# Performance work log

Measured on AMD Instinct MI355X. Metric: run time of the kernel, lower is better.

The kernel has to match this reference:

```python
import jax, jax.numpy as jnp
import numpy as np

FEAT_DIM = 2048
H_DIM = 1024
N = 8192  # num_obj (tree nodes in pre-order traversal order)


def setup_inputs() -> dict:
    key = jax.random.key(0)
    ks = jax.random.split(key, 5)
    features = jax.random.normal(ks[0], (N, FEAT_DIM), dtype=jnp.float32)
    # block_orthogonal init approximated by scaled gaussian (same math at runtime)
    Wx = jax.random.normal(ks[1], (4 * H_DIM, FEAT_DIM), dtype=jnp.float32) / np.sqrt(FEAT_DIM)
    Wh = jax.random.normal(ks[2], (4 * H_DIM, H_DIM), dtype=jnp.float32) / np.sqrt(H_DIM)
    bx = jnp.zeros((4 * H_DIM,), dtype=jnp.float32)
    # iofuh bias: forget-gate block [2h:3h] filled with 1.0
    bh = jnp.zeros((4 * H_DIM,), dtype=jnp.float32).at[2 * H_DIM:3 * H_DIM].set(1.0)
    # binary tree in pre-order-compatible (topological) order: parent of t is (t-1)//2 < t; root = -1
    t = jnp.arange(N)
    parent_idx = jnp.where(t == 0, -1, (t - 1) // 2).astype(jnp.int32)
    root_c = jax.random.normal(ks[3], (1, H_DIM), dtype=jnp.float32)
    root_h = jax.random.normal(ks[4], (1, H_DIM), dtype=jnp.float32)
    return {"features": features, "Wx": Wx, "bx": bx, "Wh": Wh, "bh": bh,
            "parent_idx": parent_idx, "root_c": root_c, "root_h": root_h}


def reference(features, Wx, bx, Wh, bh, parent_idx, root_c, root_h):
    # Precompute the input projection for ALL nodes with one big GEMM
    # (the original does this per-node; math is identical).
    xproj = features @ Wx.T + (bx + bh)  # [N, 4H]
    WhT = Wh.T  # [H, 4H]
    # state buffers; slot 0 holds the root state, slot t+1 holds node t's state
    h_buf = jnp.concatenate([root_h, jnp.zeros((N, H_DIM), features.dtype)], axis=0)  # [N+1, H]
    c_buf = jnp.concatenate([root_c, jnp.zeros((N, H_DIM), features.dtype)], axis=0)

    def step(carry, inp):
        h_buf, c_buf = carry
        t, p, xp = inp
        hp = h_buf[p + 1]  # parent hidden [H]
        cp = c_buf[p + 1]  # parent cell   [H]
        iofu = xp + hp @ WhT  # [4H]
        i, o, f, u = jnp.split(iofu, 4)
        i = jax.nn.sigmoid(i)
        o = jax.nn.sigmoid(o)
        f = jax.nn.sigmoid(f)
        u = jnp.tanh(u)
        c = i * u + f * cp
        h = o * jnp.tanh(c)
        h_buf = h_buf.at[t + 1].set(h)
        c_buf = c_buf.at[t + 1].set(c)
        return (h_buf, c_buf), h

    ts = jnp.arange(N)
    (_, _), hidden = jax.lax.scan(step, (h_buf, c_buf), (ts, parent_idx, xproj))
    return hidden  # [N, H] == treelstm_io.hidden rows in traversal order
```

## Files before the change

kernel.cpp:

```cpp
#include <hip/hip_runtime.h>
#include <hip/hip_fp16.h>
#include <math.h>

#define FEAT 2048
#define HD 1024
#define FH 4096
#define NN 8192

using s16x8 = __attribute__((ext_vector_type(8))) short;
using f32x4 = __attribute__((ext_vector_type(4))) float;

#define GLOBAL_AS __attribute__((address_space(1)))
#define LDS_AS __attribute__((address_space(3)))

__device__ __forceinline__ void gload_lds16(const void* g, void* l) {
    __builtin_amdgcn_global_load_lds((const GLOBAL_AS unsigned int*)g,
                                     (LDS_AS unsigned int*)l, 16, 0, 0);
}

__device__ __forceinline__ unsigned short f2bf(float f) {
    union { float f; unsigned u; } v; v.f = f;
    unsigned r = v.u + 0x7FFFu + ((v.u >> 16) & 1u);
    return (unsigned short)(r >> 16);
}

__device__ __forceinline__ float fast_sig(float x) { return 1.0f / (1.0f + __expf(-x)); }
__device__ __forceinline__ float fast_tanh(float x) {
    float ax = fabsf(x);
    float e = __expf(2.0f * ax);
    float r = 1.0f - 2.0f / (e + 1.0f);
    return copysignf(r, x);
}

__global__ __launch_bounds__(256) void convert_all_kernel(
    const float* __restrict__ feat, const float* __restrict__ Wx,
    const float* __restrict__ Wh, unsigned short* __restrict__ feat_b,
    unsigned short* __restrict__ Wx_b, unsigned short* __restrict__ Wh_b,
    const float* __restrict__ root_h, const float* __restrict__ root_c,
    unsigned short* __restrict__ h_buf, float* __restrict__ c_buf)
{
    const size_t g = (size_t)blockIdx.x * 256 + threadIdx.x;
    if (g < HD) { h_buf[g] = f2bf(root_h[g]); c_buf[g] = root_c[g]; }

    const size_t n1 = (size_t)NN * FEAT;
    const size_t n2 = n1 + (size_t)FH * FEAT;
    size_t i = g * 8;
    const float* s; unsigned short* d;
    if (i < n1)      { s = feat + i;        d = feat_b + i; }
    else if (i < n2) { s = Wx + (i - n1);   d = Wx_b + (i - n1); }
    else             { s = Wh + (i - n2);   d = Wh_b + (i - n2); }
    float4 a = *(const float4*)s;
    float4 b = *(const float4*)(s + 4);
    unsigned short r[8] = {f2bf(a.x), f2bf(a.y), f2bf(a.z), f2bf(a.w),
                           f2bf(b.x), f2bf(b.y), f2bf(b.z), f2bf(b.w)};
    *(s16x8*)d = *(const s16x8*)r;
}

__global__ __launch_bounds__(512, 2) void xproj_8ph(
    const unsigned short* __restrict__ Ab,
    const unsigned short* __restrict__ Bb,
    const float* __restrict__ bx, const float* __restrict__ bh,
    __half* __restrict__ xproj)
{
    __shared__ char lds[131072];
    const int tid = threadIdx.x;
    const int wid = tid >> 6;
    const int lane = tid & 63;
    const int wr = wid >> 2;
    const int wc = wid & 3;
    const int bm = blockIdx.x * 256;
    const int bn = blockIdx.y * 256;
    const int fr = lane & 15;
    const int fq = lane >> 4;

    const int srow = tid >> 3;
    const int sslot = (tid & 7) ^ (srow & 7);
    const unsigned short* gA[4];
    const unsigned short* gB[4];
    #pragma unroll
    for (int q = 0; q < 4; ++q) {
        gA[q] = Ab + (size_t)(bm + q * 64 + srow) * FEAT + sslot * 8;
        gB[q] = Bb + (size_t)(bn + q * 64 + srow) * FEAT + sslot * 8;
    }
    const int ldsoff = tid * 16;

    f32x4 acc[8][4];
    #pragma unroll
    for (int i = 0; i < 8; ++i)
        #pragma unroll
        for (int j = 0; j < 4; ++j) { f32x4 z = {0.f, 0.f, 0.f, 0.f}; acc[i][j] = z; }

    #pragma unroll
    for (int q = 0; q < 4; ++q) {
        gload_lds16(gA[q], lds + q * 8192 + ldsoff);
        gload_lds16(gB[q], lds + 32768 + q * 8192 + ldsoff);
    }

    for (int t = 0; t < 32; ++t) {
        const int d = t & 1;
        const char* LA = lds + d * 65536;
        const char* LB = LA + 32768;
        char* SA = lds + (d ^ 1) * 65536;
        char* SB = SA + 32768;
        const int knext = (t + 1) * 64;

        asm volatile("s_waitcnt vmcnt(0)" ::: "memory");
        __builtin_amdgcn_s_barrier();

        #pragma unroll
        for (int kk = 0; kk < 2; ++kk) {
            const int kbyte = kk * 64 + fq * 16;
            s16x8 aF[8], bF[4];
            #pragma unroll
            for (int i = 0; i < 8; ++i) {
                const int row = wr * 128 + i * 16 + fr;
                aF[i] = *(const s16x8*)(LA + row * 128 + (kbyte ^ ((row & 7) << 4)));
            }
            #pragma unroll
            for (int j = 0; j < 4; ++j) {
                const int row = wc * 64 + j * 16 + fr;
                bF[j] = *(const s16x8*)(LB + row * 128 + (kbyte ^ ((row & 7) << 4)));
            }
            if (t < 31) {
                if (kk == 0) {
                    #pragma unroll
                    for (int q = 0; q < 4; ++q)
                        gload_lds16(gA[q] + knext, SA + q * 8192 + ldsoff);
                } else {
                    #pragma unroll
                    for (int q = 0; q < 4; ++q)
                        gload_lds16(gB[q] + knext, SB + q * 8192 + ldsoff);
                }
            }
            __builtin_amdgcn_s_setprio(1);
            #pragma unroll
            for (int i = 0; i < 8; ++i)
                #pragma unroll
                for (int j = 0; j < 4; ++j)
                    acc[i][j] = __builtin_amdgcn_mfma_f32_16x16x32_bf16(
                        aF[i], bF[j], acc[i][j], 0, 0, 0);
            __builtin_amdgcn_s_setprio(0);
        }
    }

    __builtin_amdgcn_s_barrier();
    char* W = lds + wid * 16384;
    #pragma unroll
    for (int j = 0; j < 4; ++j) {
        const int c_loc = j * 16 + fr;
        const int col = bn + wc * 64 + c_loc;
        const float bias = bx[col] + bh[col];
        #pragma unroll
        for (int i = 0; i < 8; ++i) {
            #pragma unroll
            for (int reg = 0; reg < 4; ++reg) {
                const int r_loc = i * 16 + fq * 4 + reg;
                const int byteo = r_loc * 128 +
                    ((((c_loc >> 3) ^ (r_loc & 7)) << 4)) + (c_loc & 7) * 2;
                *(__half*)(W + byteo) = __float2half_rn(acc[i][j][reg] + bias);
            }
        }
    }
    asm volatile("s_waitcnt lgkmcnt(0)" ::: "memory");
    #pragma unroll
    for (int k = 0; k < 16; ++k) {
        const int f = k * 64 + lane;
        const int r_loc = f >> 3;
        const int cchunk = f & 7;
        const s16x8 v = *(const s16x8*)(W + r_loc * 128 +
                                        ((cchunk ^ (r_loc & 7)) << 4));
        const int grow = bm + wr * 128 + r_loc;
        const int gcol = bn + wc * 64 + cchunk * 8;
        *(s16x8*)((unsigned short*)xproj + (size_t)grow * FH + gcol) = v;
    }
}

template<int BM>
__global__ __launch_bounds__(512, 2) void level_kk(
    const __half* __restrict__ xproj, const unsigned short* __restrict__ Whb,
    int start, int prevstart, unsigned short* __restrict__ h_buf,
    float* __restrict__ c_buf, float* __restrict__ out)
{
    constexpr int MR = BM / 32;
    constexpr int ABYTES = BM * 128;
    constexpr int BUF = ABYTES + 32768;
    __shared__ char lds[2 * BUF];
    const int tid = threadIdx.x;
    const int wid = tid >> 6, lane = tid & 63;
    const int wr = wid >> 2, wc = wid & 3;
    const int fr = lane & 15, fq = lane >> 4;
    const int t0 = start + blockIdx.x * BM;
    const int jg0 = blockIdx.y * 64;

    const int srow = tid >> 3;
    const int sslot = (tid & 7) ^ (srow & 7);
    const unsigned short* gA[BM / 64];
    #pragma unroll
    for (int q = 0; q < BM / 64; ++q) {
        const int rg = blockIdx.x * BM + q * 64 + srow;
        gA[q] = h_buf + (size_t)(prevstart + (rg >> 1) + 1) * HD + sslot * 8;
    }
    const unsigned short* gB[4];
    #pragma unroll
    for (int q = 0; q < 4; ++q) {
        const int r = q * 64 + srow;
        const int whrow = ((r >> 4) & 3) * 1024 + jg0 + ((r >> 6) * 16) + (r & 15);
        gB[q] = Whb + (size_t)whrow * HD + sslot * 8;
    }
    const int ldsoff = tid * 16;

    f32x4 acc[MR][4];
    #pragma unroll
    for (int i = 0; i < MR; ++i)
        #pragma unroll
        for (int j = 0; j < 4; ++j) { f32x4 z = {0.f, 0.f, 0.f, 0.f}; acc[i][j] = z; }

    #pragma unroll
    for (int q = 0; q < BM / 64; ++q)
        gload_lds16(gA[q], lds + q * 8192 + ldsoff);
    #pragma unroll
    for (int q = 0; q < 4; ++q)
        gload_lds16(gB[q], lds + ABYTES + q * 8192 + ldsoff);

    for (int t = 0; t < 16; ++t) {
        const char* LA = lds + (t & 1) * BUF;
        const char* LB = LA + ABYTES;
        char* SA = lds + ((t & 1) ^ 1) * BUF;
        char* SB = SA + ABYTES;
        const int knext = (t + 1) * 64;

        asm volatile("s_waitcnt vmcnt(0)" ::: "memory");
        __builtin_amdgcn_s_barrier();

        #pragma unroll
        for (int kk = 0; kk < 2; ++kk) {
            const int kbyte = kk * 64 + fq * 16;
            s16x8 aF[MR], bF[4];
            #pragma unroll
            for (int i = 0; i < MR; ++i) {
                const int row = wr * (BM / 2) + i * 16 + fr;
                aF[i] = *(const s16x8*)(LA + row * 128 + (kbyte ^ ((row & 7) << 4)));
            }
            #pragma unroll
            for (int j = 0; j < 4; ++j) {
                const int row = wc * 64 + j * 16 + fr;
                bF[j] = *(const s16x8*)(LB + row * 128 + (kbyte ^ ((row & 7) << 4)));
            }
            if (t < 15) {
                if (kk == 0) {
                    #pragma unroll
                    for (int q = 0; q < BM / 64; ++q)
                        gload_lds16(gA[q] + knext, SA + q * 8192 + ldsoff);
                } else {
                    #pragma unroll
                    for (int q = 0; q < 4; ++q)
                        gload_lds16(gB[q] + knext, SB + q * 8192 + ldsoff);
                }
            }
            __builtin_amdgcn_s_setprio(1);
            #pragma unroll
            for (int i = 0; i < MR; ++i)
                #pragma unroll
                for (int j = 0; j < 4; ++j)
                    acc[i][j] = __builtin_amdgcn_mfma_f32_16x16x32_bf16(
                        aF[i], bF[j], acc[i][j], 0, 0, 0);
            __builtin_amdgcn_s_setprio(0);
        }
    }

    const int col = jg0 + wc * 16 + fr;
    #pragma unroll
    for (int i = 0; i < MR; ++i) {
        #pragma unroll
        for (int reg = 0; reg < 4; ++reg) {
            const int t = t0 + wr * (BM / 2) + i * 16 + fq * 4 + reg;
            const int p = (t - 1) >> 1;
            const size_t xb = (size_t)t * FH + col;
            const float gi = acc[i][0][reg] + __half2float(xproj[xb]);
            const float go = acc[i][1][reg] + __half2float(xproj[xb + HD]);
            const float gf = acc[i][2][reg] + __half2float(xproj[xb + 2 * HD]);
            const float gu = acc[i][3][reg] + __half2float(xproj[xb + 3 * HD]);
            const float cp = c_buf[(size_t)(p + 1) * HD + col];
            const float c = fast_sig(gi) * fast_tanh(gu) + fast_sig(gf) * cp;
            const float h = fast_sig(go) * fast_tanh(c);
            c_buf[(size_t)(t + 1) * HD + col] = c;
            h_buf[(size_t)(t + 1) * HD + col] = f2bf(h);
            out[(size_t)t * HD + col] = h;
        }
    }
}

__device__ __forceinline__ void level_epilogue(
    f32x4 (&acc)[4][4], const __half* __restrict__ xproj,
    const int* __restrict__ parent, unsigned short* __restrict__ h_buf,
    float* __restrict__ c_buf, float* __restrict__ out,
    int t0, int lim, int wm, int col, int fq)
{
    #pragma unroll
    for (int i = 0; i < 4; ++i) {
        #pragma unroll
        for (int reg = 0; reg < 4; ++reg) {
            const int t = t0 + wm + i * 16 + fq * 4 + reg;
            if (t < lim) {
                const int p = parent[t];
                const size_t xb = (size_t)t * FH + col;
                const float gi = acc[i][0][reg] + __half2float(xproj[xb]);
                const float go = acc[i][1][reg] + __half2float(xproj[xb + HD]);
                const float gf = acc[i][2][reg] + __half2float(xproj[xb + 2 * HD]);
                const float gu = acc[i][3][reg] + __half2float(xproj[xb + 3 * HD]);
                const float cp = c_buf[(size_t)(p + 1) * HD + col];
                const float c = fast_sig(gi) * fast_tanh(gu) + fast_sig(gf) * cp;
                const float h = fast_sig(go) * fast_tanh(c);
                c_buf[(size_t)(t + 1) * HD + col] = c;
                h_buf[(size_t)(t + 1) * HD + col] = f2bf(h);
                out[(size_t)t * HD + col] = h;
            }
        }
    }
}

__device__ __forceinline__ void bk128_issue(
    const unsigned short* const (&gA)[8], const unsigned short* const (&gB)[8],
    int k0, unsigned short* As, unsigned short* Bs, int wbase)
{
    #pragma unroll
    for (int q = 0; q < 8; ++q) {
        gload_lds16(gA[q] + k0, (char*)As + q * 4096 + wbase);
        gload_lds16(gB[q] + k0, (char*)Bs + q * 4096 + wbase);
    }
}

__device__ __forceinline__ void bk128_compute(
    const unsigned short* As, const unsigned short* Bs,
    f32x4 (&acc)[4][4], int wm, int wn16, int fr, int fkb)
{
    #pragma unroll
    for (int kk = 0; kk < 4; ++kk) {
        s16x8 aF[4], bF[4];
        #pragma unroll
        for (int i = 0; i < 4; ++i) {
            const int r = wm + i * 16 + fr;
            const int byteIn = (kk * 64 + fkb) ^ ((r & 7) << 4);
            aF[i] = *(const s16x8*)((const char*)As + r * 256 + byteIn);
        }
        #pragma unroll
        for (int g = 0; g < 4; ++g) {
            const int r = g * 32 + wn16 + fr;
            const int byteIn = (kk * 64 + fkb) ^ ((r & 7) << 4);
            bF[g] = *(const s16x8*)((const char*)Bs + r * 256 + byteIn);
        }
        #pragma unroll
        for (int i = 0; i < 4; ++i)
            #pragma unroll
            for (int g = 0; g < 4; ++g)
                acc[i][g] = __builtin_amdgcn_mfma_f32_16x16x32_bf16(aF[i], bF[g], acc[i][g], 0, 0, 0);
    }
}

__global__ __launch_bounds__(256) void level_bk128_dbuf(
    const __half* __restrict__ xproj, const unsigned short* __restrict__ Whb,
    const int* __restrict__ parent, unsigned short* __restrict__ h_buf,
    float* __restrict__ c_buf, float* __restrict__ out,
    int start, int count)
{
    __shared__ unsigned short As0[128 * 128];
    __shared__ unsigned short Bs0[128 * 128];
    __shared__ unsigned short As1[128 * 128];
    __shared__ unsigned short Bs1[128 * 128];
    const int tid = threadIdx.x;
    const int wid = tid >> 6;
    const int lane = tid & 63;
    const int t0 = start + blockIdx.x * 128;
    const int jg0 = blockIdx.y * 32;
    const int lim = start + count;
    const int wm = (wid & 1) * 64;
    const int wn16 = (wid >> 1) * 16;
    const int wbase = wid * 1024;
    const int srow_b = tid >> 4;
    const int rowbyte = (tid & 15) * 16;

    const unsigned short* gA[8];
    const unsigned short* gB[8];
    #pragma unroll
    for (int q = 0; q < 8; ++q) {
        const int r = q * 16 + srow_b;
        const int sk = (rowbyte ^ ((r & 7) << 4)) >> 1;
        const int tA = min(t0 + r, lim - 1);
        gA[q] = h_buf + (size_t)(parent[tA] + 1) * HD + sk;
        const int whrow = ((r >> 5) << 10) + jg0 + (r & 31);
        gB[q] = Whb + (size_t)whrow * HD + sk;
    }

    f32x4 acc[4][4];
    #pragma unroll
    for (int i = 0; i < 4; ++i)
        #pragma unroll
        for (int g = 0; g < 4; ++g) { f32x4 z = {0.f, 0.f, 0.f, 0.f}; acc[i][g] = z; }

    const int fr = lane & 15;
    const int fkb = (lane >> 4) * 16;

    bk128_issue(gA, gB, 0, As0, Bs0, wbase);
    #pragma unroll
    for (int t = 0; t < 8; ++t) {
        unsigned short* curA = (t & 1) ? As1 : As0;
        unsigned short* curB = (t & 1) ? Bs1 : Bs0;
        unsigned short* nxtA = (t & 1) ? As0 : As1;
        unsigned short* nxtB = (t & 1) ? Bs0 : Bs1;
        if (t < 7) {
            bk128_issue(gA, gB, (t + 1) * 128, nxtA, nxtB, wbase);
            asm volatile("s_waitcnt vmcnt(16)" ::: "memory");
        } else {
            asm volatile("s_waitcnt vmcnt(0)" ::: "memory");
        }
        __builtin_amdgcn_s_barrier();
        __builtin_amdgcn_sched_barrier(0);
        bk128_compute(curA, curB, acc, wm, wn16, fr, fkb);
        __builtin_amdgcn_sched_barrier(0);
        __builtin_amdgcn_s_barrier();
    }

    level_epilogue(acc, xproj, parent, h_buf, c_buf, out,
                   t0, lim, wm, jg0 + wn16 + fr, lane >> 4);
}

extern "C" void kernel_launch(void* const* d_in, const int* in_sizes, int n_in,
                              void* d_out, int out_size, void* d_ws, size_t ws_size,
                              hipStream_t stream) {
    const float* feat   = (const float*)d_in[0];
    const float* Wx     = (const float*)d_in[1];
    const float* bx     = (const float*)d_in[2];
    const float* Wh     = (const float*)d_in[3];
    const float* bh     = (const float*)d_in[4];
    const int*   parent = (const int*)d_in[5];
    const float* root_c = (const float*)d_in[6];
    const float* root_h = (const float*)d_in[7];
    float* out = (float*)d_out;

    char* ws = (char*)d_ws;
    __half* xproj = (__half*)ws;                        ws += (size_t)NN * FH * 2;
    float* c_buf = (float*)ws;                          ws += (size_t)(NN + 1) * HD * 4;
    unsigned short* feat_b = (unsigned short*)ws;       ws += (size_t)NN * FEAT * 2;
    unsigned short* Wx_b = (unsigned short*)ws;         ws += (size_t)FH * FEAT * 2;
    unsigned short* Wh_b = (unsigned short*)ws;         ws += (size_t)FH * HD * 2;
    unsigned short* h_buf = (unsigned short*)ws;        ws += (size_t)(NN + 1) * HD * 2;

    const size_t ntot = (size_t)NN * FEAT + (size_t)FH * FEAT + (size_t)FH * HD;
    convert_all_kernel<<<(unsigned)(ntot / 8 / 256), 256, 0, stream>>>(
        feat, Wx, Wh, feat_b, Wx_b, Wh_b, root_h, root_c, h_buf, c_buf);

    dim3 g1(NN / 256, FH / 256);
    xproj_8ph<<<g1, 512, 0, stream>>>(feat_b, Wx_b, bx, bh, xproj);

    for (int start = 0, sz = 1; sz <= 512; start += sz, sz *= 2) {
        dim3 g2((sz + 127) / 128, HD / 32);
        level_bk128_dbuf<<<g2, 256, 0, stream>>>(
            xproj, Wh_b, parent, h_buf, c_buf, out, start, sz);
    }

    dim3 gl(16, 16);
    level_kk<64><<<gl, 512, 0, stream>>>(xproj, Wh_b, 1023, 511,
                                         h_buf, c_buf, out);
    level_kk<128><<<gl, 512, 0, stream>>>(xproj, Wh_b, 2047, 1023,
                                          h_buf, c_buf, out);
    level_kk<256><<<gl, 512, 0, stream>>>(xproj, Wh_b, 4095, 2047,
                                          h_buf, c_buf, out);

    dim3 g3(1, HD / 32);
    level_bk128_dbuf<<<g3, 256, 0, stream>>>(
        xproj, Wh_b, parent, h_buf, c_buf, out, 8191, 1);
}
```

Before: 435.1 us.

## Fuse small tree levels into one persistent kernel with atomic level flags

Replaces the ten separate per-level launches for levels 0-9 with a single 224-block kernel. Blocks are assigned to levels and spin on per-level atomic done counters (acquire/release at agent scope) before reading the parent states. This removes launch gaps and tail serialization between the tiny levels. It relies on all 224 blocks being co-resident to avoid deadlock, and spinning blocks occupy CUs while they wait.

```diff
diff --git a/kernel.cpp b/kernel.cpp
--- a/kernel.cpp
+++ b/kernel.cpp
@@ -37,10 +37,12 @@
     const float* __restrict__ Wh, unsigned short* __restrict__ feat_b,
     unsigned short* __restrict__ Wx_b, unsigned short* __restrict__ Wh_b,
     const float* __restrict__ root_h, const float* __restrict__ root_c,
-    unsigned short* __restrict__ h_buf, float* __restrict__ c_buf)
+    unsigned short* __restrict__ h_buf, float* __restrict__ c_buf,
+    int* __restrict__ done)
 {
     const size_t g = (size_t)blockIdx.x * 256 + threadIdx.x;
     if (g < HD) { h_buf[g] = f2bf(root_h[g]); c_buf[g] = root_c[g]; }
+    if (g < 16) done[g] = 0;
 
     const size_t n1 = (size_t)NN * FEAT;
     const size_t n2 = n1 + (size_t)FH * FEAT;
@@ -175,6 +177,147 @@
     }
 }
 
+__global__ __launch_bounds__(512, 2) void levels_fused_small(
+    const __half* __restrict__ xproj, const unsigned short* __restrict__ Whb,
+    unsigned short* __restrict__ h_buf, float* __restrict__ c_buf,
+    float* __restrict__ out, int* __restrict__ done)
+{
+    constexpr int MR = 4;
+    constexpr int ABYTES = 128 * 128;
+    constexpr int BUF = ABYTES + 32768;
+    __shared__ char lds[2 * BUF];
+    const int bid = blockIdx.x;
+    int lvl, nb;
+    if (bid < 128)      { lvl = bid >> 4; nb = 0; }
+    else if (bid < 160) { lvl = 8;        nb = (bid - 128) >> 4; }
+    else                { lvl = 9;        nb = (bid - 160) >> 4; }
+    const int jg0 = (bid & 15) * 64;
+    const int start = (1 << lvl) - 1;
+    const int cnt = 1 << lvl;
+    const int lim = start + cnt;
+    const int t0 = start + nb * 128;
+
+    if (lvl > 0) {
+        if (threadIdx.x == 0) {
+            const int need = (lvl <= 8) ? 16 : 32;
+            while (__hip_atomic_load(done + (lvl - 1), __ATOMIC_ACQUIRE,
+                                     __HIP_MEMORY_SCOPE_AGENT) < need)
+                __builtin_amdgcn_s_sleep(8);
+        }
+        __syncthreads();
+    }
+
+    const int tid = threadIdx.x;
+    const int wid = tid >> 6, lane = tid & 63;
+    const int wr = wid >> 2, wc = wid & 3;
+    const int fr = lane & 15, fq = lane >> 4;
+
+    const int srow = tid >> 3;
+    const int sslot = (tid & 7) ^ (srow & 7);
+    const unsigned short* gA[2];
+    #pragma unroll
+    for (int q = 0; q < 2; ++q) {
+        const int rg = min(nb * 128 + q * 64 + srow, cnt - 1);
+        const int arow = ((start + rg - 1) >> 1) + 1;
+        gA[q] = h_buf + (size_t)arow * HD + sslot * 8;
+    }
+    const unsigned short* gB[4];
+    #pragma unroll
+    for (int q = 0; q < 4; ++q) {
+        const int r = q * 64 + srow;
+        const int whrow = ((r >> 4) & 3) * 1024 + jg0 + ((r >> 6) * 16) + (r & 15);
+        gB[q] = Whb + (size_t)whrow * HD + sslot * 8;
+    }
+    const int ldsoff = tid * 16;
+
+    f32x4 acc[MR][4];
+    #pragma unroll
+    for (int i = 0; i < MR; ++i)
+        #pragma unroll
+        for (int j = 0; j < 4; ++j) { f32x4 z = {0.f, 0.f, 0.f, 0.f}; acc[i][j] = z; }
+
+    #pragma unroll
+    for (int q = 0; q < 2; ++q)
+        gload_lds16(gA[q], lds + q * 8192 + ldsoff);
+    #pragma unroll
+    for (int q = 0; q < 4; ++q)
+        gload_lds16(gB[q], lds + ABYTES + q * 8192 + ldsoff);
+
+    for (int t = 0; t < 16; ++t) {
+        const char* LA = lds + (t & 1) * BUF;
+        const char* LB = LA + ABYTES;
+        char* SA = lds + ((t & 1) ^ 1) * BUF;
+        char* SB = SA + ABYTES;
+        const int knext = (t + 1) * 64;
+
+        asm volatile("s_waitcnt vmcnt(0)" ::: "memory");
+        __builtin_amdgcn_s_barrier();
+
+        #pragma unroll
+        for (int kk = 0; kk < 2; ++kk) {
+            const int kbyte = kk * 64 + fq * 16;
+            s16x8 aF[MR], bF[4];
+            #pragma unroll
+            for (int i = 0; i < MR; ++i) {
+                const int row = wr * 64 + i * 16 + fr;
+                aF[i] = *(const s16x8*)(LA + row * 128 + (kbyte ^ ((row & 7) << 4)));
+            }
+            #pragma unroll
+            for (int j = 0; j < 4; ++j) {
+                const int row = wc * 64 + j * 16 + fr;
+                bF[j] = *(const s16x8*)(LB + row * 128 + (kbyte ^ ((row & 7) << 4)));
+            }
+            if (t < 15) {
+                if (kk == 0) {
+                    #pragma unroll
+                    for (int q = 0; q < 2; ++q)
+                        gload_lds16(gA[q] + knext, SA + q * 8192 + ldsoff);
+                } else {
+                    #pragma unroll
+                    for (int q = 0; q < 4; ++q)
+                        gload_lds16(gB[q] + knext, SB + q * 8192 + ldsoff);
+                }
+            }
+            __builtin_amdgcn_s_setprio(1);
+            #pragma unroll
+            for (int i = 0; i < MR; ++i)
+                #pragma unroll
+                for (int j = 0; j < 4; ++j)
+                    acc[i][j] = __builtin_amdgcn_mfma_f32_16x16x32_bf16(
+                        aF[i], bF[j], acc[i][j], 0, 0, 0);
+            __builtin_amdgcn_s_setprio(0);
+        }
+    }
+
+    const int col = jg0 + wc * 16 + fr;
+    #pragma unroll
+    for (int i = 0; i < MR; ++i) {
+        #pragma unroll
+        for (int reg = 0; reg < 4; ++reg) {
+            const int t = t0 + wr * 64 + i * 16 + fq * 4 + reg;
+            if (t < lim) {
+                const int prow = ((t - 1) >> 1) + 1;
+                const size_t xb = (size_t)t * FH + col;
+                const float gi = acc[i][0][reg] + __half2float(xproj[xb]);
+                const float go = acc[i][1][reg] + __half2float(xproj[xb + HD]);
+                const float gf = acc[i][2][reg] + __half2float(xproj[xb + 2 * HD]);
+                const float gu = acc[i][3][reg] + __half2float(xproj[xb + 3 * HD]);
+                const float cp = c_buf[(size_t)prow * HD + col];
+                const float c = fast_sig(gi) * fast_tanh(gu) + fast_sig(gf) * cp;
+                const float h = fast_sig(go) * fast_tanh(c);
+                c_buf[(size_t)(t + 1) * HD + col] = c;
+                h_buf[(size_t)(t + 1) * HD + col] = f2bf(h);
+                out[(size_t)t * HD + col] = h;
+            }
+        }
+    }
+
+    __syncthreads();
+    if (threadIdx.x == 0)
+        __hip_atomic_fetch_add(done + lvl, 1, __ATOMIC_RELEASE,
+                               __HIP_MEMORY_SCOPE_AGENT);
+}
+
 template<int BM>
 __global__ __launch_bounds__(512, 2) void level_kk(
     const __half* __restrict__ xproj, const unsigned short* __restrict__ Whb,
@@ -286,35 +429,6 @@
             c_buf[(size_t)(t + 1) * HD + col] = c;
             h_buf[(size_t)(t + 1) * HD + col] = f2bf(h);
             out[(size_t)t * HD + col] = h;
-        }
-    }
-}
-
-__device__ __forceinline__ void level_epilogue(
-    f32x4 (&acc)[4][4], const __half* __restrict__ xproj,
-    const int* __restrict__ parent, unsigned short* __restrict__ h_buf,
-    float* __restrict__ c_buf, float* __restrict__ out,
-    int t0, int lim, int wm, int col, int fq)
-{
-    #pragma unroll
-    for (int i = 0; i < 4; ++i) {
-        #pragma unroll
-        for (int reg = 0; reg < 4; ++reg) {
-            const int t = t0 + wm + i * 16 + fq * 4 + reg;
-            if (t < lim) {
-                const int p = parent[t];
-                const size_t xb = (size_t)t * FH + col;
-                const float gi = acc[i][0][reg] + __half2float(xproj[xb]);
-                const float go = acc[i][1][reg] + __half2float(xproj[xb + HD]);
-                const float gf = acc[i][2][reg] + __half2float(xproj[xb + 2 * HD]);
-                const float gu = acc[i][3][reg] + __half2float(xproj[xb + 3 * HD]);
-                const float cp = c_buf[(size_t)(p + 1) * HD + col];
-                const float c = fast_sig(gi) * fast_tanh(gu) + fast_sig(gf) * cp;
-                const float h = fast_sig(go) * fast_tanh(c);
-                c_buf[(size_t)(t + 1) * HD + col] = c;
-                h_buf[(size_t)(t + 1) * HD + col] = f2bf(h);
-                out[(size_t)t * HD + col] = h;
-            }
         }
     }
 }
@@ -420,8 +534,29 @@
         __builtin_amdgcn_s_barrier();
     }
 
-    level_epilogue(acc, xproj, parent, h_buf, c_buf, out,
-                   t0, lim, wm, jg0 + wn16 + fr, lane >> 4);
+    const int col = jg0 + wn16 + fr;
+    const int fq = lane >> 4;
+    #pragma unroll
+    for (int i = 0; i < 4; ++i) {
+        #pragma unroll
+        for (int reg = 0; reg < 4; ++reg) {
+            const int t = t0 + wm + i * 16 + fq * 4 + reg;
+            if (t < lim) {
+                const int p = parent[t];
+                const size_t xb = (size_t)t * FH + col;
+                const float gi = acc[i][0][reg] + __half2float(xproj[xb]);
+                const float go = acc[i][1][reg] + __half2float(xproj[xb + HD]);
+                const float gf = acc[i][2][reg] + __half2float(xproj[xb + 2 * HD]);
+                const float gu = acc[i][3][reg] + __half2float(xproj[xb + 3 * HD]);
+                const float cp = c_buf[(size_t)(p + 1) * HD + col];
+                const float c = fast_sig(gi) * fast_tanh(gu) + fast_sig(gf) * cp;
+                const float h = fast_sig(go) * fast_tanh(c);
+                c_buf[(size_t)(t + 1) * HD + col] = c;
+                h_buf[(size_t)(t + 1) * HD + col] = f2bf(h);
+                out[(size_t)t * HD + col] = h;
+            }
+        }
+    }
 }
 
 extern "C" void kernel_launch(void* const* d_in, const int* in_sizes, int n_in,
@@ -444,19 +579,17 @@
     unsigned short* Wx_b = (unsigned short*)ws;         ws += (size_t)FH * FEAT * 2;
     unsigned short* Wh_b = (unsigned short*)ws;         ws += (size_t)FH * HD * 2;
     unsigned short* h_buf = (unsigned short*)ws;        ws += (size_t)(NN + 1) * HD * 2;
+    int* done = (int*)ws;                               ws += 256;
 
     const size_t ntot = (size_t)NN * FEAT + (size_t)FH * FEAT + (size_t)FH * HD;
     convert_all_kernel<<<(unsigned)(ntot / 8 / 256), 256, 0, stream>>>(
-        feat, Wx, Wh, feat_b, Wx_b, Wh_b, root_h, root_c, h_buf, c_buf);
+        feat, Wx, Wh, feat_b, Wx_b, Wh_b, root_h, root_c, h_buf, c_buf, done);
 
     dim3 g1(NN / 256, FH / 256);
     xproj_8ph<<<g1, 512, 0, stream>>>(feat_b, Wx_b, bx, bh, xproj);
 
-    for (int start = 0, sz = 1; sz <= 512; start += sz, sz *= 2) {
-        dim3 g2((sz + 127) / 128, HD / 32);
-        level_bk128_dbuf<<<g2, 256, 0, stream>>>(
-            xproj, Wh_b, parent, h_buf, c_buf, out, start, sz);
-    }
+    levels_fused_small<<<224, 512, 0, stream>>>(
+        xproj, Wh_b, h_buf, c_buf, out, done);
 
     dim3 gl(16, 16);
     level_kk<64><<<gl, 512, 0, stream>>>(xproj, Wh_b, 1023, 511,
```

Measured after the change: 715.2 us. +64.4%, slower.
